# Kernel optimization log

Hardware: AMD Instinct MI355X
Metric: run time of the kernel (lower is better)

Reference implementation:

```python
import jax, jax.numpy as jnp
import numpy as np
import itertools

# LeViT-style Attention config (matches init_kwargs)
DIM = 256
KD = 32          # key_dim
H = 8            # num_heads
AR = 4           # attn_ratio
RES = 14
N = RES * RES    # 196 tokens
D = AR * KD      # per-head value dim = 128
DH = D * H       # 1024
NHKD = KD * H    # 256
HID = DH + 2 * NHKD  # 1536 = qkv width
EPS = 1e-5
SCALE = KD ** -0.5
BATCH = 256


def _bias_idxs():
    # Same construction as the torch module: index into table of unique abs offsets.
    points = list(itertools.product(range(RES), range(RES)))
    offs = {}
    idxs = []
    for p1 in points:
        for p2 in points:
            o = (abs(p1[0] - p2[0]), abs(p1[1] - p2[1]))
            if o not in offs:
                offs[o] = len(offs)
            idxs.append(offs[o])
    return np.asarray(idxs, dtype=np.int32).reshape(N, N), len(offs)


def _bn(x, g, b):
    # BatchNorm1d in training mode over the flattened (B*N, F) batch dim.
    mu = x.mean(axis=0)
    var = jnp.var(x, axis=0)  # biased, as torch BN uses for normalization
    return (x - mu) * jax.lax.rsqrt(var + EPS) * g + b


def setup_inputs() -> dict:
    key = jax.random.key(0)
    ks = jax.random.split(key, 8)
    idxs_np, n_off = _bias_idxs()  # n_off == 196 for RES=14
    x = jax.random.normal(ks[0], (BATCH, N, DIM), dtype=jnp.float32)
    Wqkv = jax.random.normal(ks[1], (HID, DIM), dtype=jnp.float32) * 0.02
    g1 = 1.0 + 0.1 * jax.random.normal(ks[2], (HID,), dtype=jnp.float32)
    b1 = 0.1 * jax.random.normal(ks[3], (HID,), dtype=jnp.float32)
    # init is zeros in the module; use small randn so the bias path is exercised
    bias_table = 0.1 * jax.random.normal(ks[4], (H, n_off), dtype=jnp.float32)
    Wproj = jax.random.normal(ks[5], (DIM, DH), dtype=jnp.float32) * 0.02
    # bn_weight_init=0 in module; use nonzero so output/grads are nontrivial
    g2 = 1.0 + 0.1 * jax.random.normal(ks[6], (DIM,), dtype=jnp.float32)
    b2 = 0.1 * jax.random.normal(ks[7], (DIM,), dtype=jnp.float32)
    return {
        "x": x, "Wqkv": Wqkv, "g1": g1, "b1": b1,
        "bias_table": bias_table, "Wproj": Wproj, "g2": g2, "b2": b2,
        "idxs": jnp.asarray(idxs_np),
    }


def reference(x, Wqkv, g1, b1, bias_table, Wproj, g2, b2, idxs):
    B, Ntok, C = x.shape
    # qkv = Linear_BN(x): bias-free linear then BN over flattened (B*N, HID)
    h = jnp.einsum('bnc,hc->bnh', x, Wqkv)
    h = _bn(h.reshape(B * Ntok, HID), g1, b1).reshape(B, Ntok, H, -1)
    q = h[..., :KD].transpose(0, 2, 1, 3)            # (B,H,N,KD)
    k = h[..., KD:2 * KD].transpose(0, 2, 1, 3)      # (B,H,N,KD)
    v = h[..., 2 * KD:].transpose(0, 2, 1, 3)        # (B,H,N,D)
    bias = bias_table[:, idxs]                       # (H,N,N) relative-position bias gather
    attn = jnp.einsum('bhnd,bhmd->bhnm', q, k) * SCALE + bias
    attn = jax.nn.softmax(attn, axis=-1)
    o = jnp.einsum('bhnm,bhmd->bhnd', attn, v)
    o = o.transpose(0, 2, 1, 3).reshape(B, Ntok, DH)
    # proj = Hardswish -> Linear_BN(dh, dim)
    o = o * jnp.clip(o + 3.0, 0.0, 6.0) / 6.0
    o = jnp.einsum('bnd,cd->bnc', o, Wproj)
    o = _bn(o.reshape(B * Ntok, C), g2, b2).reshape(B, Ntok, C)
    return o
```

## Files before the change

kernel.cpp:

```cpp
#include <hip/hip_runtime.h>

typedef _Float16 f16;
typedef __attribute__((ext_vector_type(8))) _Float16 half8;
typedef __attribute__((ext_vector_type(4))) _Float16 half4;
typedef __attribute__((ext_vector_type(4))) float   f4;

#define NTOK   196
#define MROWS  50176
#define HIDN   1536
#define HPC    192
#define DHD    1024
#define EPSV   1e-5f
#define SCALEV 0.17677669529663687f

__device__ inline int swz8(int row) { return (((row & 7) ^ ((row >> 3) & 7))) * 8; }

__global__ void cvt_f32_f16(const float* __restrict__ src, f16* __restrict__ dst, int n4)
{
    int i = blockIdx.x * blockDim.x + threadIdx.x;
    if (i < n4) {
        float4 v = *(const float4*)&src[i * 4];
        half4 h = { (f16)v.x, (f16)v.y, (f16)v.z, (f16)v.w };
        *(half4*)&dst[i * 4] = h;
    }
}

__global__ __launch_bounds__(256) void gemm1_qkv(
    const f16* __restrict__ A, const f16* __restrict__ B,
    f16* __restrict__ C, float* __restrict__ gsum, float* __restrict__ gsq)
{
    const int K = 256, ldc = HIDN;
    __shared__ f16 As[128][40];
    __shared__ f16 Bs[128][40];
    __shared__ float ssum[128], ssq[128];

    const int t = threadIdx.x;
    const int m0 = blockIdx.x * 128, n0 = blockIdx.y * 128;
    const int wid = t >> 6, lane = t & 63, quad = lane >> 4, lm = lane & 15;
    const int wm = (wid >> 1) * 64, wn = (wid & 1) * 64;

    f4 acc[4][4] = {};

    for (int k0 = 0; k0 < K; k0 += 32) {
        #pragma unroll
        for (int s = 0; s < 2; ++s) {
            int ch = t + s * 256;
            int r = ch >> 2, c8 = (ch & 3) * 8;
            *(half8*)&As[r][c8] = *(const half8*)&A[(long)(m0 + r) * K + k0 + c8];
            *(half8*)&Bs[r][c8] = *(const half8*)&B[(long)(n0 + r) * K + k0 + c8];
        }
        __syncthreads();
        half8 a[4], b[4];
        #pragma unroll
        for (int i = 0; i < 4; ++i) a[i] = *(const half8*)&As[wm + i*16 + lm][quad*8];
        #pragma unroll
        for (int j = 0; j < 4; ++j) b[j] = *(const half8*)&Bs[wn + j*16 + lm][quad*8];
        #pragma unroll
        for (int i = 0; i < 4; ++i)
            #pragma unroll
            for (int j = 0; j < 4; ++j)
                acc[i][j] = __builtin_amdgcn_mfma_f32_16x16x32_f16(a[i], b[j], acc[i][j], 0, 0, 0);
        __syncthreads();
    }

    if (t < 128) { ssum[t] = 0.f; ssq[t] = 0.f; }
    __syncthreads();

    #pragma unroll
    for (int j = 0; j < 4; ++j) {
        int nl = wn + j*16 + lm;
        float psum = 0.f, psq = 0.f;
        #pragma unroll
        for (int i = 0; i < 4; ++i) {
            #pragma unroll
            for (int r = 0; r < 4; ++r) {
                int ml = wm + i*16 + quad*4 + r;
                float v = acc[i][j][r];
                f16 uh = (f16)v;
                float vb = (float)uh;
                C[(long)(m0 + ml) * ldc + n0 + nl] = uh;
                psum += vb; psq += vb * vb;
            }
        }
        atomicAdd(&ssum[nl], psum);
        atomicAdd(&ssq[nl], psq);
    }
    __syncthreads();
    if (t < 128) {
        atomicAdd(&gsum[n0 + t], ssum[t]);
        atomicAdd(&gsq[n0 + t],  ssq[t]);
    }
}

__global__ __launch_bounds__(256) void gemm2_proj(
    const f16* __restrict__ A, const f16* __restrict__ B,
    float* __restrict__ C, float* __restrict__ gsum, float* __restrict__ gsq)
{
    const int K = 1024, ldc = 256;
    __shared__ f16 As[128][40];
    __shared__ f16 Bs[128][40];
    __shared__ float ssum[128], ssq[128];

    const int t = threadIdx.x;
    const int m0 = blockIdx.x * 128, n0 = blockIdx.y * 128;
    const int wid = t >> 6, lane = t & 63, quad = lane >> 4, lm = lane & 15;
    const int wm = (wid >> 1) * 64, wn = (wid & 1) * 64;

    f4 acc[4][4] = {};

    for (int k0 = 0; k0 < K; k0 += 32) {
        #pragma unroll
        for (int s = 0; s < 2; ++s) {
            int ch = t + s * 256;
            int r = ch >> 2, c8 = (ch & 3) * 8;
            *(half8*)&As[r][c8] = *(const half8*)&A[(long)(m0 + r) * K + k0 + c8];
            *(half8*)&Bs[r][c8] = *(const half8*)&B[(long)(n0 + r) * K + k0 + c8];
        }
        __syncthreads();
        half8 a[4], b[4];
        #pragma unroll
        for (int i = 0; i < 4; ++i) a[i] = *(const half8*)&As[wm + i*16 + lm][quad*8];
        #pragma unroll
        for (int j = 0; j < 4; ++j) b[j] = *(const half8*)&Bs[wn + j*16 + lm][quad*8];
        #pragma unroll
        for (int i = 0; i < 4; ++i)
            #pragma unroll
            for (int j = 0; j < 4; ++j)
                acc[i][j] = __builtin_amdgcn_mfma_f32_16x16x32_f16(a[i], b[j], acc[i][j], 0, 0, 0);
        __syncthreads();
    }

    if (t < 128) { ssum[t] = 0.f; ssq[t] = 0.f; }
    __syncthreads();

    #pragma unroll
    for (int j = 0; j < 4; ++j) {
        int nl = wn + j*16 + lm;
        float psum = 0.f, psq = 0.f;
        #pragma unroll
        for (int i = 0; i < 4; ++i) {
            #pragma unroll
            for (int r = 0; r < 4; ++r) {
                int ml = wm + i*16 + quad*4 + r;
                float v = acc[i][j][r];
                C[(long)(m0 + ml) * ldc + n0 + nl] = v;
                psum += v; psq += v * v;
            }
        }
        atomicAdd(&ssum[nl], psum);
        atomicAdd(&ssq[nl], psq);
    }
    __syncthreads();
    if (t < 128) {
        atomicAdd(&gsum[n0 + t], ssum[t]);
        atomicAdd(&gsq[n0 + t],  ssq[t]);
    }
}

__global__ void bn_fin(const float* __restrict__ gsum, const float* __restrict__ gsq,
                       const float* __restrict__ g, const float* __restrict__ b,
                       float* __restrict__ a_out, float* __restrict__ s_out, int nch)
{
    int c = blockIdx.x * blockDim.x + threadIdx.x;
    if (c >= nch) return;
    float inv  = 1.f / (float)MROWS;
    float mean = gsum[c] * inv;
    float var  = gsq[c] * inv - mean * mean;
    float a    = g[c] * rsqrtf(var + EPSV);
    a_out[c] = a;
    s_out[c] = b[c] - mean * a;
}

__global__ __launch_bounds__(512) void attn_kernel(
    const f16* __restrict__ hbuf, const float* __restrict__ a1, const float* __restrict__ s1,
    const float* __restrict__ bias_table, const int* __restrict__ idxs,
    f16* __restrict__ obuf)
{
    __shared__ f16   qs[208][32];
    __shared__ f16   ks[208][32];
    __shared__ f16   vT[128][256];
    __shared__ f16   ps[8][16][256];
    __shared__ float af[192], sf[192];
    __shared__ float biasr[196];

    const int t  = threadIdx.x;
    const int bb = blockIdx.x >> 3;
    const int hh = blockIdx.x & 7;
    const int wid = t >> 6, lane = t & 63, quad = lane >> 4, lm = lane & 15;

    if (t < 192) { af[t] = a1[hh * HPC + t]; sf[t] = s1[hh * HPC + t]; }
    if (t < 196) { biasr[t] = bias_table[hh * 196 + t]; }
    half8 z8 = {};
    for (int i = t; i < 4096; i += 512) *(half8*)&vT[i >> 5][(i & 31) * 8] = z8;
    for (int i = t; i < 4096; i += 512) *(half8*)&ps[i >> 9][(i >> 5) & 15][(i & 31) * 8] = z8;
    for (int i = t; i < 12 * 32; i += 512) { qs[196 + (i >> 5)][i & 31] = (f16)0.f;
                                             ks[196 + (i >> 5)][i & 31] = (f16)0.f; }
    __syncthreads();

    {
        int t8 = t & 7;
        for (int rr = t >> 3; rr < NTOK; rr += 64) {
            const f16* hrow = hbuf + (long)(bb * NTOK + rr) * HIDN + hh * HPC;
            int sr = swz8(rr);
            #pragma unroll
            for (int cc = 0; cc < 3; ++cc) {
                int cb = (t8 + cc * 8) * 8;
                half8 raw = *(const half8*)(hrow + cb);
                f16 ov[8];
                #pragma unroll
                for (int e = 0; e < 8; ++e)
                    ov[e] = (f16)((float)raw[e] * af[cb + e] + sf[cb + e]);
                if (cb < 32) {
                    #pragma unroll
                    for (int e = 0; e < 8; ++e) qs[rr][(cb + e + sr) & 31] = ov[e];
                } else if (cb < 64) {
                    #pragma unroll
                    for (int e = 0; e < 8; ++e) ks[rr][(cb - 32 + e + sr) & 31] = ov[e];
                } else {
                    #pragma unroll
                    for (int e = 0; e < 8; ++e) {
                        int c = cb - 64 + e;
                        vT[c][(rr + swz8(c)) & 255] = ov[e];
                    }
                }
            }
        }
    }
    __syncthreads();

    const int nmt = (wid + 8 < 13) ? 2 : 1;
    half8 ap[2][7];

    for (int pass = 0; pass < nmt; ++pass) {
        const int mt = wid + pass * 8;
        int qrowA = mt * 16 + lm;
        half8 aq = *(const half8*)&qs[qrowA][(quad * 8 + swz8(qrowA)) & 31];
        f4 sreg[13];
        #pragma unroll
        for (int nt = 0; nt < 13; ++nt) {
            int krow = nt * 16 + lm;
            half8 bk = *(const half8*)&ks[krow][(quad * 8 + swz8(krow)) & 31];
            f4 z = {};
            sreg[nt] = __builtin_amdgcn_mfma_f32_16x16x32_f16(aq, bk, z, 0, 0, 0);
        }
        #pragma unroll
        for (int nt = 0; nt < 13; ++nt) {
            int kc = nt * 16 + lm;
            int ksafe = kc < 196 ? kc : 195;
            #pragma unroll
            for (int r = 0; r < 4; ++r) {
                int qrow = mt * 16 + quad * 4 + r;
                int qsafe = qrow < 196 ? qrow : 195;
                float bias_v = biasr[idxs[qsafe * 196 + ksafe]];
                float sv = sreg[nt][r] * SCALEV + bias_v;
                sreg[nt][r] = (kc < 196) ? sv : -1e30f;
            }
        }
        float rinv[4];
        #pragma unroll
        for (int r = 0; r < 4; ++r) {
            float m = sreg[0][r];
            #pragma unroll
            for (int nt = 1; nt < 13; ++nt) m = fmaxf(m, sreg[nt][r]);
            #pragma unroll
            for (int d = 1; d < 16; d <<= 1) m = fmaxf(m, __shfl_xor(m, d));
            float s = 0.f;
            #pragma unroll
            for (int nt = 0; nt < 13; ++nt) {
                float e = __expf(sreg[nt][r] - m);
                sreg[nt][r] = e;
                s += e;
            }
            #pragma unroll
            for (int d = 1; d < 16; d <<= 1) s += __shfl_xor(s, d);
            rinv[r] = 1.f / s;
        }
        #pragma unroll
        for (int nt = 0; nt < 13; ++nt)
            #pragma unroll
            for (int r = 0; r < 4; ++r) {
                int q = quad * 4 + r;
                ps[wid][q][(nt * 16 + lm + swz8(q)) & 255] = (f16)(sreg[nt][r] * rinv[r]);
            }
        #pragma unroll
        for (int k7 = 0; k7 < 7; ++k7)
            ap[pass][k7] = *(const half8*)&ps[wid][lm][(k7 * 32 + quad * 8 + swz8(lm)) & 255];
    }

    #pragma unroll
    for (int ct = 0; ct < 8; ++ct) {
        int c = ct * 16 + lm;
        int sc = swz8(c);
        f4 oa0 = {}, oa1 = {};
        #pragma unroll
        for (int k7 = 0; k7 < 7; ++k7) {
            half8 bv = *(const half8*)&vT[c][(k7 * 32 + quad * 8 + sc) & 255];
            oa0 = __builtin_amdgcn_mfma_f32_16x16x32_f16(ap[0][k7], bv, oa0, 0, 0, 0);
            if (nmt == 2)
                oa1 = __builtin_amdgcn_mfma_f32_16x16x32_f16(ap[1][k7], bv, oa1, 0, 0, 0);
        }
        #pragma unroll
        for (int r = 0; r < 4; ++r) {
            int qrow = wid * 16 + quad * 4 + r;
            if (qrow < 196) {
                float v  = oa0[r];
                float hs = v * fminf(fmaxf(v + 3.f, 0.f), 6.f) * (1.f / 6.f);
                obuf[(long)(bb * NTOK + qrow) * DHD + hh * 128 + c] = (f16)hs;
            }
        }
        if (nmt == 2) {
            #pragma unroll
            for (int r = 0; r < 4; ++r) {
                int qrow = (wid + 8) * 16 + quad * 4 + r;
                if (qrow < 196) {
                    float v  = oa1[r];
                    float hs = v * fminf(fmaxf(v + 3.f, 0.f), 6.f) * (1.f / 6.f);
                    obuf[(long)(bb * NTOK + qrow) * DHD + hh * 128 + c] = (f16)hs;
                }
            }
        }
    }
}

__global__ __launch_bounds__(256) void bn_apply(
    float* __restrict__ out, const float* __restrict__ a2, const float* __restrict__ s2)
{
    __shared__ float aL[256], sL[256];
    int t = threadIdx.x;
    aL[t] = a2[t]; sL[t] = s2[t];
    __syncthreads();
    long total = (long)MROWS * 256 / 4;
    for (long i = (long)blockIdx.x * 256 + t; i < total; i += (long)gridDim.x * 256) {
        float4 v = *(float4*)&out[i * 4];
        int cb = (int)((i * 4) & 255);
        v.x = v.x * aL[cb + 0] + sL[cb + 0];
        v.y = v.y * aL[cb + 1] + sL[cb + 1];
        v.z = v.z * aL[cb + 2] + sL[cb + 2];
        v.w = v.w * aL[cb + 3] + sL[cb + 3];
        *(float4*)&out[i * 4] = v;
    }
}

extern "C" void kernel_launch(void* const* d_in, const int* in_sizes, int n_in,
                              void* d_out, int out_size, void* d_ws, size_t ws_size,
                              hipStream_t stream)
{
    (void)in_sizes; (void)n_in; (void)out_size; (void)ws_size;
    const float* x          = (const float*)d_in[0];
    const float* Wqkv       = (const float*)d_in[1];
    const float* g1         = (const float*)d_in[2];
    const float* b1         = (const float*)d_in[3];
    const float* bias_table = (const float*)d_in[4];
    const float* Wproj      = (const float*)d_in[5];
    const float* g2         = (const float*)d_in[6];
    const float* b2         = (const float*)d_in[7];
    const int*   idxs       = (const int*)d_in[8];
    float*       out        = (float*)d_out;

    char* ws = (char*)d_ws;
    f16* hbuf = (f16*)ws;
    f16* obuf = (f16*)(ws + 154140672LL);
    f16* xh   = (f16*)(ws + 154140672LL);
    f16* wqh  = (f16*)(ws + 154140672LL + 25690112LL);
    f16* wph  = (f16*)ws;
    float* stats = (float*)(ws + 256901120LL);
    float* gsum1 = stats;            float* gsq1 = stats + 1536;
    float* gsum2 = stats + 3072;     float* gsq2 = stats + 3328;
    float* a1 = stats + 3584;        float* s1 = a1 + 1536;
    float* a2 = s1 + 1536;           float* s2 = a2 + 256;

    hipMemsetAsync(stats, 0, 3584 * sizeof(float), stream);

    cvt_f32_f16<<<12544, 256, 0, stream>>>(x, xh, 3211264);
    cvt_f32_f16<<<384,   256, 0, stream>>>(Wqkv, wqh, 98304);

    gemm1_qkv<<<dim3(392, 12), 256, 0, stream>>>(xh, wqh, hbuf, gsum1, gsq1);
    bn_fin<<<6, 256, 0, stream>>>(gsum1, gsq1, g1, b1, a1, s1, 1536);

    attn_kernel<<<2048, 512, 0, stream>>>(hbuf, a1, s1, bias_table, idxs, obuf);

    cvt_f32_f16<<<256, 256, 0, stream>>>(Wproj, wph, 65536);

    gemm2_proj<<<dim3(392, 2), 256, 0, stream>>>(obuf, wph, out, gsum2, gsq2);
    bn_fin<<<1, 256, 0, stream>>>(gsum2, gsq2, g2, b2, a2, s2, 256);

    bn_apply<<<1024, 256, 0, stream>>>(out, a2, s2);
}
```

Baseline: 485.7 us.

## Use direct global-to-LDS loads in GEMMs and precompute dense f16 bias table

```diff
diff --git a/kernel.cpp b/kernel.cpp
--- a/kernel.cpp
+++ b/kernel.cpp
@@ -13,6 +13,10 @@
 #define EPSV   1e-5f
 #define SCALEV 0.17677669529663687f
 
+#define GLD16(gp, lp) __builtin_amdgcn_global_load_lds( \
+    (const __attribute__((address_space(1))) unsigned int*)(gp), \
+    (__attribute__((address_space(3))) unsigned int*)(lp), 16, 0, 0)
+
 __device__ inline int swz8(int row) { return (((row & 7) ^ ((row >> 3) & 7))) * 8; }
 
 __global__ void cvt_f32_f16(const float* __restrict__ src, f16* __restrict__ dst, int n4)
@@ -25,13 +29,24 @@
     }
 }
 
+__global__ void build_bias(const float* __restrict__ bt, const int* __restrict__ idxs,
+                           f16* __restrict__ bf)
+{
+    int i = blockIdx.x * 256 + threadIdx.x;
+    if (i >= 8 * 208 * 224) return;
+    int k = i % 224, q = (i / 224) % 208, h = i / (224 * 208);
+    float v = -30000.f;
+    if (q < NTOK && k < NTOK) v = bt[h * NTOK + idxs[q * NTOK + k]];
+    bf[i] = (f16)v;
+}
+
 __global__ __launch_bounds__(256) void gemm1_qkv(
     const f16* __restrict__ A, const f16* __restrict__ B,
     f16* __restrict__ C, float* __restrict__ gsum, float* __restrict__ gsq)
 {
     const int K = 256, ldc = HIDN;
-    __shared__ f16 As[128][40];
-    __shared__ f16 Bs[128][40];
+    __shared__ f16 As[128 * 32];
+    __shared__ f16 Bs[128 * 32];
     __shared__ float ssum[128], ssq[128];
 
     const int t = threadIdx.x;
@@ -39,22 +54,27 @@
     const int wid = t >> 6, lane = t & 63, quad = lane >> 4, lm = lane & 15;
     const int wm = (wid >> 1) * 64, wn = (wid & 1) * 64;
 
+    const int lr = lane >> 2, lc = (lane & 3) * 8;
+    f16* As0 = &As[(wid * 2 + 0) * 512];
+    f16* As1 = &As[(wid * 2 + 1) * 512];
+    f16* Bs0 = &Bs[(wid * 2 + 0) * 512];
+    f16* Bs1 = &Bs[(wid * 2 + 1) * 512];
+    const f16* Ab = A + (long)(m0 + wid * 32 + lr) * K + lc;
+    const f16* Bb = B + (long)(n0 + wid * 32 + lr) * K + lc;
+
     f4 acc[4][4] = {};
 
     for (int k0 = 0; k0 < K; k0 += 32) {
-        #pragma unroll
-        for (int s = 0; s < 2; ++s) {
-            int ch = t + s * 256;
-            int r = ch >> 2, c8 = (ch & 3) * 8;
-            *(half8*)&As[r][c8] = *(const half8*)&A[(long)(m0 + r) * K + k0 + c8];
-            *(half8*)&Bs[r][c8] = *(const half8*)&B[(long)(n0 + r) * K + k0 + c8];
-        }
+        GLD16(Ab + k0,          As0);
+        GLD16(Ab + 16 * K + k0, As1);
+        GLD16(Bb + k0,          Bs0);
+        GLD16(Bb + 16 * K + k0, Bs1);
         __syncthreads();
         half8 a[4], b[4];
         #pragma unroll
-        for (int i = 0; i < 4; ++i) a[i] = *(const half8*)&As[wm + i*16 + lm][quad*8];
-        #pragma unroll
-        for (int j = 0; j < 4; ++j) b[j] = *(const half8*)&Bs[wn + j*16 + lm][quad*8];
+        for (int i = 0; i < 4; ++i) a[i] = *(const half8*)&As[(wm + i*16 + lm) * 32 + quad * 8];
+        #pragma unroll
+        for (int j = 0; j < 4; ++j) b[j] = *(const half8*)&Bs[(wn + j*16 + lm) * 32 + quad * 8];
         #pragma unroll
         for (int i = 0; i < 4; ++i)
             #pragma unroll
@@ -97,8 +117,8 @@
     float* __restrict__ C, float* __restrict__ gsum, float* __restrict__ gsq)
 {
     const int K = 1024, ldc = 256;
-    __shared__ f16 As[128][40];
-    __shared__ f16 Bs[128][40];
+    __shared__ f16 As[128 * 32];
+    __shared__ f16 Bs[128 * 32];
     __shared__ float ssum[128], ssq[128];
 
     const int t = threadIdx.x;
@@ -106,22 +126,27 @@
     const int wid = t >> 6, lane = t & 63, quad = lane >> 4, lm = lane & 15;
     const int wm = (wid >> 1) * 64, wn = (wid & 1) * 64;
 
+    const int lr = lane >> 2, lc = (lane & 3) * 8;
+    f16* As0 = &As[(wid * 2 + 0) * 512];
+    f16* As1 = &As[(wid * 2 + 1) * 512];
+    f16* Bs0 = &Bs[(wid * 2 + 0) * 512];
+    f16* Bs1 = &Bs[(wid * 2 + 1) * 512];
+    const f16* Ab = A + (long)(m0 + wid * 32 + lr) * K + lc;
+    const f16* Bb = B + (long)(n0 + wid * 32 + lr) * K + lc;
+
     f4 acc[4][4] = {};
 
     for (int k0 = 0; k0 < K; k0 += 32) {
-        #pragma unroll
-        for (int s = 0; s < 2; ++s) {
-            int ch = t + s * 256;
-            int r = ch >> 2, c8 = (ch & 3) * 8;
-            *(half8*)&As[r][c8] = *(const half8*)&A[(long)(m0 + r) * K + k0 + c8];
-            *(half8*)&Bs[r][c8] = *(const half8*)&B[(long)(n0 + r) * K + k0 + c8];
-        }
+        GLD16(Ab + k0,          As0);
+        GLD16(Ab + 16 * K + k0, As1);
+        GLD16(Bb + k0,          Bs0);
+        GLD16(Bb + 16 * K + k0, Bs1);
         __syncthreads();
         half8 a[4], b[4];
         #pragma unroll
-        for (int i = 0; i < 4; ++i) a[i] = *(const half8*)&As[wm + i*16 + lm][quad*8];
-        #pragma unroll
-        for (int j = 0; j < 4; ++j) b[j] = *(const half8*)&Bs[wn + j*16 + lm][quad*8];
+        for (int i = 0; i < 4; ++i) a[i] = *(const half8*)&As[(wm + i*16 + lm) * 32 + quad * 8];
+        #pragma unroll
+        for (int j = 0; j < 4; ++j) b[j] = *(const half8*)&Bs[(wn + j*16 + lm) * 32 + quad * 8];
         #pragma unroll
         for (int i = 0; i < 4; ++i)
             #pragma unroll
@@ -173,15 +198,13 @@
 
 __global__ __launch_bounds__(512) void attn_kernel(
     const f16* __restrict__ hbuf, const float* __restrict__ a1, const float* __restrict__ s1,
-    const float* __restrict__ bias_table, const int* __restrict__ idxs,
-    f16* __restrict__ obuf)
+    const f16* __restrict__ bf, f16* __restrict__ obuf)
 {
     __shared__ f16   qs[208][32];
     __shared__ f16   ks[208][32];
     __shared__ f16   vT[128][256];
     __shared__ f16   ps[8][16][256];
     __shared__ float af[192], sf[192];
-    __shared__ float biasr[196];
 
     const int t  = threadIdx.x;
     const int bb = blockIdx.x >> 3;
@@ -189,7 +212,6 @@
     const int wid = t >> 6, lane = t & 63, quad = lane >> 4, lm = lane & 15;
 
     if (t < 192) { af[t] = a1[hh * HPC + t]; sf[t] = s1[hh * HPC + t]; }
-    if (t < 196) { biasr[t] = bias_table[hh * 196 + t]; }
     half8 z8 = {};
     for (int i = t; i < 4096; i += 512) *(half8*)&vT[i >> 5][(i & 31) * 8] = z8;
     for (int i = t; i < 4096; i += 512) *(half8*)&ps[i >> 9][(i >> 5) & 15][(i & 31) * 8] = z8;
@@ -230,6 +252,7 @@
 
     const int nmt = (wid + 8 < 13) ? 2 : 1;
     half8 ap[2][7];
+    const f16* bfh = bf + hh * 208 * 224;
 
     for (int pass = 0; pass < nmt; ++pass) {
         const int mt = wid + pass * 8;
@@ -246,14 +269,11 @@
         #pragma unroll
         for (int nt = 0; nt < 13; ++nt) {
             int kc = nt * 16 + lm;
-            int ksafe = kc < 196 ? kc : 195;
             #pragma unroll
             for (int r = 0; r < 4; ++r) {
                 int qrow = mt * 16 + quad * 4 + r;
-                int qsafe = qrow < 196 ? qrow : 195;
-                float bias_v = biasr[idxs[qsafe * 196 + ksafe]];
-                float sv = sreg[nt][r] * SCALEV + bias_v;
-                sreg[nt][r] = (kc < 196) ? sv : -1e30f;
+                float bias_v = (float)bfh[qrow * 224 + kc];
+                sreg[nt][r] = sreg[nt][r] * SCALEV + bias_v;
             }
         }
         float rinv[4];
@@ -368,16 +388,18 @@
     float* gsum2 = stats + 3072;     float* gsq2 = stats + 3328;
     float* a1 = stats + 3584;        float* s1 = a1 + 1536;
     float* a2 = s1 + 1536;           float* s2 = a2 + 256;
+    f16* bias_full = (f16*)(ws + 256901120LL + 65536LL);
 
     hipMemsetAsync(stats, 0, 3584 * sizeof(float), stream);
 
     cvt_f32_f16<<<12544, 256, 0, stream>>>(x, xh, 3211264);
     cvt_f32_f16<<<384,   256, 0, stream>>>(Wqkv, wqh, 98304);
+    build_bias<<<1456, 256, 0, stream>>>(bias_table, idxs, bias_full);
 
     gemm1_qkv<<<dim3(392, 12), 256, 0, stream>>>(xh, wqh, hbuf, gsum1, gsq1);
     bn_fin<<<6, 256, 0, stream>>>(gsum1, gsq1, g1, b1, a1, s1, 1536);
 
-    attn_kernel<<<2048, 512, 0, stream>>>(hbuf, a1, s1, bias_table, idxs, obuf);
+    attn_kernel<<<2048, 512, 0, stream>>>(hbuf, a1, s1, bias_full, obuf);
 
     cvt_f32_f16<<<256, 256, 0, stream>>>(Wproj, wph, 65536);
 
```

Measured after the change: 474.9 us. -2.2%, faster.
